# Optimization experiments

Hardware: AMD Instinct MI355X
Metric: run time of the kernel (lower is better)

## Reference

```python
import jax, jax.numpy as jnp
import numpy as np

N_HEAD = 16
HEAD_DIM = 64

def setup_inputs() -> dict:
    key = jax.random.key(0)
    k1, k2, k3 = jax.random.split(key, 3)
    B, S, D = 4, 2048, 1024
    x = jax.random.normal(k1, (B, S, D), dtype=jnp.float32)
    mask = jnp.tril(jnp.ones((S, S), dtype=bool))[None, None]  # (1,1,S,S) causal
    w_attn = jax.random.normal(k2, (D, 3 * D), dtype=jnp.float32) * (1.0 / np.sqrt(D))
    b_attn = jnp.zeros((3 * D,), dtype=jnp.float32)
    w_proj = jax.random.normal(k3, (D, D), dtype=jnp.float32) * (1.0 / np.sqrt(D))
    b_proj = jnp.zeros((D,), dtype=jnp.float32)
    return {"x": x, "mask": mask, "w_attn": w_attn, "b_attn": b_attn,
            "w_proj": w_proj, "b_proj": b_proj}

def reference(x, mask, w_attn, b_attn, w_proj, b_proj):
    B, S, D = x.shape
    H, hd = N_HEAD, HEAD_DIM
    qkv = x @ w_attn + b_attn                      # (B,S,3D)
    q, k, v = jnp.split(qkv, 3, axis=-1)
    q = q.reshape(B, S, H, hd).transpose(0, 2, 1, 3)  # (B,H,S,hd)
    k = k.reshape(B, S, H, hd).transpose(0, 2, 1, 3)
    v = v.reshape(B, S, H, hd).transpose(0, 2, 1, 3)
    scores = jnp.einsum('bhqd,bhkd->bhqk', q, k) / jnp.sqrt(jnp.float32(hd))
    scores = jnp.where(mask, scores, jnp.float32(-1e10))
    weights = jax.nn.softmax(scores, axis=-1)      # dropout is identity (deterministic=True)
    attn = jnp.einsum('bhqk,bhkd->bhqd', weights, v)
    attn = attn.transpose(0, 2, 1, 3).reshape(B, S, D)
    return attn @ w_proj + b_proj
```

## Files before the change

### kernel.cpp

```cpp
#include <hip/hip_runtime.h>
#include <hip/hip_bf16.h>
#include <stdint.h>


typedef uint16_t u16;
typedef __bf16 bf16x8 __attribute__((ext_vector_type(8)));
typedef __bf16 bf16x4 __attribute__((ext_vector_type(4)));
typedef short s16x4 __attribute__((ext_vector_type(4)));
typedef float f32x4 __attribute__((ext_vector_type(4)));

#define S_LEN 2048
#define DMODEL 1024
#define NHEAD 16
#define HDIM 64
#define MTOT 8192
#define NQKV 3072

__device__ __forceinline__ u16 f2bf(float f) {
    union { float f; uint32_t u; } v; v.f = f;
    uint32_t u = v.u;
    return (u16)((u + 0x7fffu + ((u >> 16) & 1u)) >> 16);
}

__device__ __forceinline__ s16x4 bits4(bf16x4 v) {
    union { bf16x4 b; s16x4 s; } u; u.b = v; return u.s;
}

__device__ __forceinline__ f32x4 mfma16(bf16x4 a, bf16x4 b, f32x4 c) {
    return __builtin_amdgcn_mfma_f32_16x16x16bf16_1k(bits4(a), bits4(b), c, 0, 0, 0);
}

__device__ __forceinline__ void async_load16(const void* g, void* l) {
    __builtin_amdgcn_global_load_lds(
        (__attribute__((address_space(1))) void*)g,
        (__attribute__((address_space(3))) void*)l,
        16, 0, 0);
}

__global__ void convert_x_kernel(const float4* __restrict__ in, ushort4* __restrict__ out, int n4) {
    int i = blockIdx.x * 256 + threadIdx.x;
    if (i < n4) {
        float4 f = in[i];
        ushort4 o;
        o.x = f2bf(f.x); o.y = f2bf(f.y); o.z = f2bf(f.z); o.w = f2bf(f.w);
        out[i] = o;
    }
}

__global__ void transpose_bf16_kernel(const float* __restrict__ in, u16* __restrict__ out, int R, int C) {
    __shared__ float tile[64][65];
    int r0 = blockIdx.y * 64, c0 = blockIdx.x * 64;
    #pragma unroll
    for (int i = 0; i < 16; ++i) {
        int idx = threadIdx.x + i * 256;
        int r = idx >> 6, c = idx & 63;
        tile[r][c] = in[(size_t)(r0 + r) * C + c0 + c];
    }
    __syncthreads();
    #pragma unroll
    for (int i = 0; i < 16; ++i) {
        int idx = threadIdx.x + i * 256;
        int c = idx >> 6, r = idx & 63;
        out[(size_t)(c0 + c) * R + r0 + r] = f2bf(tile[r][c]);
    }
}

__global__ void transpose_v_kernel(const u16* __restrict__ qkv, u16* __restrict__ vt) {
    __shared__ u16 tile[64 * 66];
    const int tid = threadIdx.x;
    const int stile = blockIdx.x, bh = blockIdx.y;
    const int b = bh >> 4, h = bh & 15;
    const u16* src = qkv + ((size_t)b * S_LEN + stile * 64) * NQKV + 2 * DMODEL + h * HDIM;
    #pragma unroll
    for (int it = 0; it < 2; ++it) {
        int item = it * 256 + tid;
        int s = item >> 3, d0 = (item & 7) * 8;
        bf16x8 v = *(const bf16x8*)(src + (size_t)s * NQKV + d0);
        const u16* vu = (const u16*)&v;
        #pragma unroll
        for (int j = 0; j < 8; ++j) tile[(d0 + j) * 66 + s] = vu[j];
    }
    __syncthreads();
    #pragma unroll
    for (int it = 0; it < 2; ++it) {
        int item = it * 256 + tid;
        int d = item >> 3, s0 = (item & 7) * 8;
        union { u16 u[8]; uint4 v; } pk;
        #pragma unroll
        for (int j = 0; j < 8; ++j) pk.u[j] = tile[d * 66 + s0 + j];
        *(uint4*)(vt + ((size_t)bh * 64 + d) * S_LEN + stile * 64 + s0) = pk.v;
    }
}

template<bool OUT_BF16>
__global__ __launch_bounds__(256, 2) void gemm_bt(
    const u16* __restrict__ A, const u16* __restrict__ Bt,
    const float* __restrict__ bias, void* __restrict__ C,
    int M, int N, int K)
{
    __shared__ __attribute__((aligned(16))) u16 As[128 * 32];
    __shared__ __attribute__((aligned(16))) u16 Bs[128 * 32];
    const int tid = threadIdx.x;
    const int wave = tid >> 6, lane = tid & 63;
    const int l15 = lane & 15, q4 = lane >> 4;
    const int wm = wave >> 1, wn = wave & 1;

    const int gx = gridDim.x, gy = gridDim.y;
    int bid = (int)blockIdx.y * gx + (int)blockIdx.x;
    const int PANEL = 8;
    int panel = bid / (PANEL * gy);
    int within = bid - panel * (PANEL * gy);
    int mb = panel * PANEL + (within % PANEL);
    int nb = within / PANEL;
    const int m0 = mb * 128, n0 = nb * 128;

    f32x4 acc[4][4] = {};

    const int srow = lane >> 2;
    const int scol = (lane & 3) * 8;

    for (int k0 = 0; k0 < K; k0 += 32) {
        #pragma unroll
        for (int q = 0; q < 2; ++q) {
            int r = wave * 32 + q * 16 + srow;
            async_load16(A  + (size_t)(m0 + r) * K + k0 + scol, As + (wave * 32 + q * 16) * 32);
            async_load16(Bt + (size_t)(n0 + r) * K + k0 + scol, Bs + (wave * 32 + q * 16) * 32);
        }
        __syncthreads();

        bf16x8 af[4], bfr[4];
        #pragma unroll
        for (int t = 0; t < 4; ++t) {
            af[t]  = *(const bf16x8*)(As + (wm * 64 + t * 16 + l15) * 32 + q4 * 8);
            bfr[t] = *(const bf16x8*)(Bs + (wn * 64 + t * 16 + l15) * 32 + q4 * 8);
        }
        #pragma unroll
        for (int tm = 0; tm < 4; ++tm)
            #pragma unroll
            for (int tn = 0; tn < 4; ++tn)
                acc[tm][tn] = __builtin_amdgcn_mfma_f32_16x16x32_bf16(af[tm], bfr[tn], acc[tm][tn], 0, 0, 0);
        __syncthreads();
    }

    #pragma unroll
    for (int tm = 0; tm < 4; ++tm) {
        int row = m0 + wm * 64 + tm * 16 + q4 * 4;
        #pragma unroll
        for (int tn = 0; tn < 4; ++tn) {
            int col = n0 + wn * 64 + tn * 16 + l15;
            float bv = bias[col];
            #pragma unroll
            for (int r2 = 0; r2 < 4; ++r2) {
                float v = acc[tm][tn][r2] + bv;
                if (OUT_BF16) ((u16*)C)[(size_t)(row + r2) * N + col] = f2bf(v);
                else          ((float*)C)[(size_t)(row + r2) * N + col] = v;
            }
        }
    }
}

__global__ __launch_bounds__(256, 4) void attn_kernel(
    const u16* __restrict__ qkv, const u16* __restrict__ vt, u16* __restrict__ out)
{
    __shared__ __attribute__((aligned(16))) u16 Ks[2][64 * 64];
    __shared__ __attribute__((aligned(16))) u16 Vs[2][64 * 64];

    const int tid = threadIdx.x;
    const int w = tid >> 6, lane = tid & 63;
    const int l15 = lane & 15, q4 = lane >> 4;
    const int qt = (int)gridDim.x - 1 - (int)blockIdx.x;
    const int bh = blockIdx.y;
    const int b = bh >> 4, h = bh & 15;
    const size_t base = (size_t)b * S_LEN;

    bf16x8 qf[2][2];
    #pragma unroll
    for (int mh = 0; mh < 2; ++mh) {
        int qrow = qt * 128 + mh * 64 + w * 16 + l15;
        #pragma unroll
        for (int kc = 0; kc < 2; ++kc) {
            bf16x8 raw = *(const bf16x8*)(qkv + (base + qrow) * (size_t)NQKV + h * HDIM + kc * 32 + q4 * 8);
            bf16x8 sc;
            #pragma unroll
            for (int j = 0; j < 8; ++j) sc[j] = (__bf16)((float)raw[j] * 0.125f);
            qf[mh][kc] = sc;
        }
    }

    bf16x4 ones4;
    #pragma unroll
    for (int j = 0; j < 4; ++j) ones4[j] = (__bf16)1.0f;

    f32x4 o0[4] = {}, o1[4] = {};
    f32x4 la0 = {}, la1 = {};

    const int srow8 = lane >> 3, schunk = lane & 7;

    #define STAGE(kt_, buf_)                                                          \
        _Pragma("unroll")                                                             \
        for (int q = 0; q < 2; ++q) {                                                 \
            int rloc = w * 16 + q * 8 + srow8;                                        \
            int sc = ((schunk ^ (rloc & 7)) * 8);                                     \
            async_load16(qkv + (base + (kt_) * 64 + rloc) * (size_t)NQKV + DMODEL     \
                             + h * HDIM + sc,                                         \
                         &Ks[buf_][(w * 16 + q * 8) * 64]);                           \
            async_load16(vt + ((size_t)bh * 64 + rloc) * S_LEN + (kt_) * 64 + sc,     \
                         &Vs[buf_][(w * 16 + q * 8) * 64]);                           \
        }

    STAGE(0, 0);

    const int ktdiag = 2 * qt;
    for (int kt = 0; kt <= ktdiag; ++kt) {
        const int buf = kt & 1;
        __syncthreads();
        STAGE(kt + 1, buf ^ 1);

        f32x4 st0[4] = {}, st1[4] = {};
        #pragma unroll
        for (int nt = 0; nt < 4; ++nt) {
            int n = nt * 16 + l15;
            #pragma unroll
            for (int kc = 0; kc < 2; ++kc) {
                int ch = (((kc * 4 + q4) ^ (n & 7)) * 8);
                bf16x8 kf = *(const bf16x8*)(&Ks[buf][n * 64 + ch]);
                st0[nt] = __builtin_amdgcn_mfma_f32_16x16x32_bf16(kf, qf[0][kc], st0[nt], 0, 0, 0);
                st1[nt] = __builtin_amdgcn_mfma_f32_16x16x32_bf16(kf, qf[1][kc], st1[nt], 0, 0, 0);
            }
        }

        if (kt == ktdiag) {
            #pragma unroll
            for (int nt = 0; nt < 4; ++nt) {
                #pragma unroll
                for (int r = 0; r < 4; ++r) {
                    int keyl = nt * 16 + q4 * 4 + r;
                    if (keyl > w * 16 + l15) st0[nt][r] = -1e30f;
                }
            }
        }

        bf16x4 pb0[4], pb1[4];
        #pragma unroll
        for (int nt = 0; nt < 4; ++nt) {
            #pragma unroll
            for (int r = 0; r < 4; ++r) {
                pb0[nt][r] = (__bf16)__expf(st0[nt][r]);
                pb1[nt][r] = (__bf16)__expf(st1[nt][r]);
            }
        }

        #pragma unroll
        for (int nt = 0; nt < 4; ++nt) {
            #pragma unroll
            for (int mt = 0; mt < 4; ++mt) {
                int row = mt * 16 + l15;
                int ch = (nt * 2 + (q4 >> 1)) ^ (row & 7);
                bf16x4 vf = *(const bf16x4*)(&Vs[buf][row * 64 + ch * 8 + (q4 & 1) * 4]);
                o0[mt] = mfma16(vf, pb0[nt], o0[mt]);
                o1[mt] = mfma16(vf, pb1[nt], o1[mt]);
            }
            la0 = mfma16(ones4, pb0[nt], la0);
            la1 = mfma16(ones4, pb1[nt], la1);
        }
    }

    {
        const int buf = (ktdiag + 1) & 1;
        __syncthreads();

        f32x4 st1[4] = {};
        #pragma unroll
        for (int nt = 0; nt < 4; ++nt) {
            int n = nt * 16 + l15;
            #pragma unroll
            for (int kc = 0; kc < 2; ++kc) {
                int ch = (((kc * 4 + q4) ^ (n & 7)) * 8);
                bf16x8 kf = *(const bf16x8*)(&Ks[buf][n * 64 + ch]);
                st1[nt] = __builtin_amdgcn_mfma_f32_16x16x32_bf16(kf, qf[1][kc], st1[nt], 0, 0, 0);
            }
        }
        bf16x4 pb1[4];
        #pragma unroll
        for (int nt = 0; nt < 4; ++nt) {
            #pragma unroll
            for (int r = 0; r < 4; ++r) {
                int keyl = nt * 16 + q4 * 4 + r;
                float s = (keyl > w * 16 + l15) ? -1e30f : st1[nt][r];
                pb1[nt][r] = (__bf16)__expf(s);
            }
        }
        #pragma unroll
        for (int nt = 0; nt < 4; ++nt) {
            #pragma unroll
            for (int mt = 0; mt < 4; ++mt) {
                int row = mt * 16 + l15;
                int ch = (nt * 2 + (q4 >> 1)) ^ (row & 7);
                bf16x4 vf = *(const bf16x4*)(&Vs[buf][row * 64 + ch * 8 + (q4 & 1) * 4]);
                o1[mt] = mfma16(vf, pb1[nt], o1[mt]);
            }
            la1 = mfma16(ones4, pb1[nt], la1);
        }
    }

    __bf16* outb = (__bf16*)out;
    float inv0 = 1.0f / la0[0], inv1 = 1.0f / la1[0];
    int row0 = qt * 128 + w * 16 + l15;
    int row1 = row0 + 64;
    #pragma unroll
    for (int mt = 0; mt < 4; ++mt) {
        #pragma unroll
        for (int r = 0; r < 4; ++r) {
            int col = h * HDIM + mt * 16 + q4 * 4 + r;
            outb[(base + row0) * (size_t)DMODEL + col] = (__bf16)(o0[mt][r] * inv0);
            outb[(base + row1) * (size_t)DMODEL + col] = (__bf16)(o1[mt][r] * inv1);
        }
    }
}

extern "C" void kernel_launch(void* const* d_in, const int* in_sizes, int n_in,
                              void* d_out, int out_size, void* d_ws, size_t ws_size,
                              hipStream_t stream) {
    const float* x      = (const float*)d_in[0];
    const float* w_attn = (const float*)d_in[2];
    const float* b_attn = (const float*)d_in[3];
    const float* w_proj = (const float*)d_in[4];
    const float* b_proj = (const float*)d_in[5];

    u16* xb   = (u16*)d_ws;
    u16* wat  = xb  + (size_t)MTOT * DMODEL;
    u16* wpt  = wat + (size_t)NQKV * DMODEL;
    u16* qkv  = wpt + (size_t)DMODEL * DMODEL;
    u16* attn = qkv + (size_t)MTOT * NQKV;
    u16* vt   = xb;

    convert_x_kernel<<<(MTOT * DMODEL / 4 + 255) / 256, 256, 0, stream>>>(
        (const float4*)x, (ushort4*)xb, MTOT * DMODEL / 4);
    transpose_bf16_kernel<<<dim3(NQKV / 64, DMODEL / 64), 256, 0, stream>>>(w_attn, wat, DMODEL, NQKV);
    transpose_bf16_kernel<<<dim3(DMODEL / 64, DMODEL / 64), 256, 0, stream>>>(w_proj, wpt, DMODEL, DMODEL);

    gemm_bt<true><<<dim3(MTOT / 128, NQKV / 128), 256, 0, stream>>>(
        xb, wat, b_attn, (void*)qkv, MTOT, NQKV, DMODEL);

    transpose_v_kernel<<<dim3(S_LEN / 64, 4 * NHEAD), 256, 0, stream>>>(qkv, vt);

    attn_kernel<<<dim3(S_LEN / 128, 4 * NHEAD), 256, 0, stream>>>(qkv, vt, attn);

    gemm_bt<false><<<dim3(MTOT / 128, DMODEL / 128), 256, 0, stream>>>(
        attn, wpt, b_proj, d_out, MTOT, DMODEL, DMODEL);
}
```

Before: 301.4 us.

## Triple-buffer attention K/V tiles, pair causal q-tiles per block, use exp2

The attention kernel now has each block process two complementary query tiles (one from the end, one from the start) so every block does the same causal work, and the grid is halved. K/V staging moves from double to triple buffering with a two-tile prefetch distance. The softmax scale folds in log2(e) so the kernel can use the hardware exp2 instruction. Output stores are vectorised to 8-byte writes, and the occupancy hints for both the GEMM and attention kernels change. The third buffer uses more LDS and the grid has fewer blocks, which may limit occupancy or leave CUs idle.

```diff
diff --git a/kernel.cpp b/kernel.cpp
--- a/kernel.cpp
+++ b/kernel.cpp
@@ -93,7 +93,7 @@
 }
 
 template<bool OUT_BF16>
-__global__ __launch_bounds__(256, 2) void gemm_bt(
+__global__ __launch_bounds__(256, 3) void gemm_bt(
     const u16* __restrict__ A, const u16* __restrict__ Bt,
     const float* __restrict__ bias, void* __restrict__ C,
     int M, int N, int K)
@@ -159,20 +159,31 @@
     }
 }
 
-__global__ __launch_bounds__(256, 4) void attn_kernel(
-    const u16* __restrict__ qkv, const u16* __restrict__ vt, u16* __restrict__ out)
+__device__ __forceinline__ void stage_tiles(
+    const u16* __restrict__ qkv, const u16* __restrict__ vt,
+    size_t base, int bh, int h, int w, int srow8, int schunk,
+    int kt, u16* __restrict__ KsB, u16* __restrict__ VsB)
 {
-    __shared__ __attribute__((aligned(16))) u16 Ks[2][64 * 64];
-    __shared__ __attribute__((aligned(16))) u16 Vs[2][64 * 64];
-
-    const int tid = threadIdx.x;
-    const int w = tid >> 6, lane = tid & 63;
+    #pragma unroll
+    for (int q = 0; q < 2; ++q) {
+        int rloc = w * 16 + q * 8 + srow8;
+        int sc = ((schunk ^ (rloc & 7)) * 8);
+        async_load16(qkv + (base + (size_t)kt * 64 + rloc) * (size_t)NQKV + DMODEL + h * HDIM + sc,
+                     KsB + (w * 16 + q * 8) * 64);
+        async_load16(vt + ((size_t)bh * 64 + rloc) * S_LEN + kt * 64 + sc,
+                     VsB + (w * 16 + q * 8) * 64);
+    }
+}
+
+__device__ __forceinline__ void attn_pass(
+    int qt, const u16* __restrict__ qkv, const u16* __restrict__ vt,
+    __bf16* __restrict__ outb, u16 (*Ks)[64 * 64], u16 (*Vs)[64 * 64],
+    int w, int lane, int bh, int h, size_t base)
+{
     const int l15 = lane & 15, q4 = lane >> 4;
-    const int qt = (int)gridDim.x - 1 - (int)blockIdx.x;
-    const int bh = blockIdx.y;
-    const int b = bh >> 4, h = bh & 15;
-    const size_t base = (size_t)b * S_LEN;
-
+    const int srow8 = lane >> 3, schunk = lane & 7;
+
+    const float QSCALE = 0.125f * 1.44269504f;
     bf16x8 qf[2][2];
     #pragma unroll
     for (int mh = 0; mh < 2; ++mh) {
@@ -182,7 +193,7 @@
             bf16x8 raw = *(const bf16x8*)(qkv + (base + qrow) * (size_t)NQKV + h * HDIM + kc * 32 + q4 * 8);
             bf16x8 sc;
             #pragma unroll
-            for (int j = 0; j < 8; ++j) sc[j] = (__bf16)((float)raw[j] * 0.125f);
+            for (int j = 0; j < 8; ++j) sc[j] = (__bf16)((float)raw[j] * QSCALE);
             qf[mh][kc] = sc;
         }
     }
@@ -194,27 +205,19 @@
     f32x4 o0[4] = {}, o1[4] = {};
     f32x4 la0 = {}, la1 = {};
 
-    const int srow8 = lane >> 3, schunk = lane & 7;
-
-    #define STAGE(kt_, buf_)                                                          \
-        _Pragma("unroll")                                                             \
-        for (int q = 0; q < 2; ++q) {                                                 \
-            int rloc = w * 16 + q * 8 + srow8;                                        \
-            int sc = ((schunk ^ (rloc & 7)) * 8);                                     \
-            async_load16(qkv + (base + (kt_) * 64 + rloc) * (size_t)NQKV + DMODEL     \
-                             + h * HDIM + sc,                                         \
-                         &Ks[buf_][(w * 16 + q * 8) * 64]);                           \
-            async_load16(vt + ((size_t)bh * 64 + rloc) * S_LEN + (kt_) * 64 + sc,     \
-                         &Vs[buf_][(w * 16 + q * 8) * 64]);                           \
-        }
-
-    STAGE(0, 0);
-
-    const int ktdiag = 2 * qt;
-    for (int kt = 0; kt <= ktdiag; ++kt) {
-        const int buf = kt & 1;
+    const int ktlast = 2 * qt + 1;
+
+    __syncthreads();
+    stage_tiles(qkv, vt, base, bh, h, w, srow8, schunk, 0, Ks[0], Vs[0]);
+    if (ktlast >= 1)
+        stage_tiles(qkv, vt, base, bh, h, w, srow8, schunk, 1, Ks[1], Vs[1]);
+
+    for (int kt = 0; kt <= 2 * qt; ++kt) {
+        const int buf = kt % 3;
         __syncthreads();
-        STAGE(kt + 1, buf ^ 1);
+        int pf = kt + 2;
+        if (pf <= ktlast)
+            stage_tiles(qkv, vt, base, bh, h, w, srow8, schunk, pf, Ks[pf % 3], Vs[pf % 3]);
 
         f32x4 st0[4] = {}, st1[4] = {};
         #pragma unroll
@@ -229,26 +232,24 @@
             }
         }
 
-        if (kt == ktdiag) {
-            #pragma unroll
-            for (int nt = 0; nt < 4; ++nt) {
+        if (kt == 2 * qt) {
+            #pragma unroll
+            for (int nt = 0; nt < 4; ++nt)
                 #pragma unroll
                 for (int r = 0; r < 4; ++r) {
                     int keyl = nt * 16 + q4 * 4 + r;
                     if (keyl > w * 16 + l15) st0[nt][r] = -1e30f;
                 }
-            }
         }
 
         bf16x4 pb0[4], pb1[4];
         #pragma unroll
-        for (int nt = 0; nt < 4; ++nt) {
+        for (int nt = 0; nt < 4; ++nt)
             #pragma unroll
             for (int r = 0; r < 4; ++r) {
-                pb0[nt][r] = (__bf16)__expf(st0[nt][r]);
-                pb1[nt][r] = (__bf16)__expf(st1[nt][r]);
-            }
-        }
+                pb0[nt][r] = (__bf16)__builtin_amdgcn_exp2f(st0[nt][r]);
+                pb1[nt][r] = (__bf16)__builtin_amdgcn_exp2f(st1[nt][r]);
+            }
 
         #pragma unroll
         for (int nt = 0; nt < 4; ++nt) {
@@ -266,7 +267,7 @@
     }
 
     {
-        const int buf = (ktdiag + 1) & 1;
+        const int buf = ktlast % 3;
         __syncthreads();
 
         f32x4 st1[4] = {};
@@ -282,14 +283,13 @@
         }
         bf16x4 pb1[4];
         #pragma unroll
-        for (int nt = 0; nt < 4; ++nt) {
+        for (int nt = 0; nt < 4; ++nt)
             #pragma unroll
             for (int r = 0; r < 4; ++r) {
                 int keyl = nt * 16 + q4 * 4 + r;
                 float s = (keyl > w * 16 + l15) ? -1e30f : st1[nt][r];
-                pb1[nt][r] = (__bf16)__expf(s);
-            }
-        }
+                pb1[nt][r] = (__bf16)__builtin_amdgcn_exp2f(s);
+            }
         #pragma unroll
         for (int nt = 0; nt < 4; ++nt) {
             #pragma unroll
@@ -303,19 +303,38 @@
         }
     }
 
-    __bf16* outb = (__bf16*)out;
     float inv0 = 1.0f / la0[0], inv1 = 1.0f / la1[0];
     int row0 = qt * 128 + w * 16 + l15;
     int row1 = row0 + 64;
     #pragma unroll
     for (int mt = 0; mt < 4; ++mt) {
+        union { __bf16 b[4]; ushort4 v; } p0, p1;
         #pragma unroll
         for (int r = 0; r < 4; ++r) {
-            int col = h * HDIM + mt * 16 + q4 * 4 + r;
-            outb[(base + row0) * (size_t)DMODEL + col] = (__bf16)(o0[mt][r] * inv0);
-            outb[(base + row1) * (size_t)DMODEL + col] = (__bf16)(o1[mt][r] * inv1);
-        }
-    }
+            p0.b[r] = (__bf16)(o0[mt][r] * inv0);
+            p1.b[r] = (__bf16)(o1[mt][r] * inv1);
+        }
+        int col = h * HDIM + mt * 16 + q4 * 4;
+        *(ushort4*)(&outb[(base + row0) * (size_t)DMODEL + col]) = p0.v;
+        *(ushort4*)(&outb[(base + row1) * (size_t)DMODEL + col]) = p1.v;
+    }
+}
+
+__global__ __launch_bounds__(256, 3) void attn_kernel(
+    const u16* __restrict__ qkv, const u16* __restrict__ vt, u16* __restrict__ out)
+{
+    __shared__ __attribute__((aligned(16))) u16 Ks[3][64 * 64];
+    __shared__ __attribute__((aligned(16))) u16 Vs[3][64 * 64];
+
+    const int tid = threadIdx.x;
+    const int w = tid >> 6, lane = tid & 63;
+    const int bh = blockIdx.y;
+    const int b = bh >> 4, h = bh & 15;
+    const size_t base = (size_t)b * S_LEN;
+    const int NT = (int)gridDim.x * 2;
+
+    attn_pass(NT - 1 - (int)blockIdx.x, qkv, vt, (__bf16*)out, Ks, Vs, w, lane, bh, h, base);
+    attn_pass((int)blockIdx.x,          qkv, vt, (__bf16*)out, Ks, Vs, w, lane, bh, h, base);
 }
 
 extern "C" void kernel_launch(void* const* d_in, const int* in_sizes, int n_in,
@@ -344,7 +363,7 @@
 
     transpose_v_kernel<<<dim3(S_LEN / 64, 4 * NHEAD), 256, 0, stream>>>(qkv, vt);
 
-    attn_kernel<<<dim3(S_LEN / 128, 4 * NHEAD), 256, 0, stream>>>(qkv, vt, attn);
+    attn_kernel<<<dim3(S_LEN / 256, 4 * NHEAD), 256, 0, stream>>>(qkv, vt, attn);
 
     gemm_bt<false><<<dim3(MTOT / 128, DMODEL / 128), 256, 0, stream>>>(
         attn, wpt, b_proj, d_out, MTOT, DMODEL, DMODEL);
```

Measured after the change: 273.7 us. -9.2%, faster.
